# Kernel optimization log

Hardware: AMD Instinct MI355X
Metric: run time of the kernel (lower is better)

## Reference

```python
import jax, jax.numpy as jnp
import numpy as np

N_NODES = 100000
N_EDGES = 1600000
N_IN = 256
N_H = 128


def setup_inputs() -> dict:
    key = jax.random.key(0)
    k1, k2, k3, k4 = jax.random.split(key, 4)
    x = jax.random.normal(k1, (N_NODES, N_IN), dtype=jnp.float32)
    edge_index = jax.random.randint(k2, (2, N_EDGES), 0, N_NODES, dtype=jnp.int64)
    # GCNConv weights (glorot-like scale) and biases
    W1 = jax.random.normal(k3, (N_IN, N_H), dtype=jnp.float32) / np.sqrt(N_IN)
    b1 = jnp.zeros((N_H,), dtype=jnp.float32)
    W2 = jax.random.normal(k4, (N_H, N_H), dtype=jnp.float32) / np.sqrt(N_H)
    b2 = jnp.zeros((N_H,), dtype=jnp.float32)
    return {"x": x, "W1": W1, "b1": b1, "W2": W2, "b2": b2, "edge_index": edge_index}


def _gcn_conv(x, W, b, row, col, n_nodes):
    """PyG GCNConv: add self-loops, symmetric norm D^-1/2 A D^-1/2, aggregate at target (col)."""
    h = x @ W  # [N, out]
    # degree including self-loop (edge_weight = 1): deg[i] = 1 + #incoming edges at target i
    deg = jnp.ones((n_nodes,), dtype=x.dtype).at[col].add(1.0)
    dinv = jax.lax.rsqrt(deg)
    # off-diagonal edges: msg j->i weighted by dinv[j]*dinv[i]
    norm = dinv[row] * dinv[col]  # [E]
    msg = h[row] * norm[:, None]  # [E, out]
    agg = jax.ops.segment_sum(msg, col, num_segments=n_nodes)
    # self-loop contribution: weight dinv[i]^2
    agg = agg + h * (dinv * dinv)[:, None]
    return agg + b


def reference(x, W1, b1, W2, b2, edge_index):
    row, col = edge_index[0], edge_index[1]
    n = x.shape[0]
    out = jax.nn.relu(_gcn_conv(x, W1, b1, row, col, n))
    out = _gcn_conv(out, W2, b2, row, col, n)
    return out
```

## Files before the change

### kernel.cpp

```cpp
#include <hip/hip_runtime.h>


#define NN 100000
#define NH 128
#define NB 196
#define SB 256

__device__ __forceinline__ float bf2f(unsigned int u) { return __uint_as_float(u << 16); }
__device__ __forceinline__ unsigned short f2bf(float f) {
    unsigned int u = __float_as_uint(f);
    u = (u + 0x7fffu + ((u >> 16) & 1u)) >> 16;
    return (unsigned short)u;
}

__device__ __forceinline__ void dma16(const void* g, void* l) {
    __builtin_amdgcn_global_load_lds(
        (const __attribute__((address_space(1))) unsigned int*)g,
        (__attribute__((address_space(3))) unsigned int*)l, 16, 0, 0);
}

__global__ __launch_bounds__(256) void k_hist(const int* __restrict__ col,
                                              int* __restrict__ blockCnt, int E, int chb) {
    __shared__ int h[NB];
    int t = threadIdx.x, blk = blockIdx.x;
    if (t < NB) h[t] = 0;
    __syncthreads();
    int s = blk * chb, en = min(E, s + chb);
    for (int e = s + t; e < en; e += 256) atomicAdd(&h[col[e] >> 9], 1);
    __syncthreads();
    if (t < NB) blockCnt[t * SB + blk] = h[t];
}

__global__ __launch_bounds__(256) void k_base(const int* __restrict__ blockCnt,
                                              int* __restrict__ base) {
    __shared__ int s[256];
    int t = threadIdx.x;
    int tot = 0;
    if (t < NB)
        for (int j = 0; j < SB; ++j) tot += blockCnt[t * SB + j];
    s[t] = tot;
    __syncthreads();
    for (int off = 1; off < 256; off <<= 1) {
        int v = (t >= off) ? s[t - off] : 0;
        __syncthreads();
        s[t] += v;
        __syncthreads();
    }
    if (t < NB) base[t] = s[t] - tot;
    if (t == NB - 1) base[NB] = s[t];
}

__global__ __launch_bounds__(256) void k_bscan(const int* __restrict__ blockCnt,
                                               const int* __restrict__ base,
                                               int* __restrict__ blockOff) {
    __shared__ int s[256];
    int t = threadIdx.x, b = blockIdx.x;
    int v = blockCnt[b * SB + t];
    s[t] = v;
    __syncthreads();
    for (int off = 1; off < 256; off <<= 1) {
        int u = (t >= off) ? s[t - off] : 0;
        __syncthreads();
        s[t] += u;
        __syncthreads();
    }
    blockOff[b * SB + t] = base[b] + s[t] - v;
}

__global__ __launch_bounds__(256) void k_scatter(const int* __restrict__ row,
                                                 const int* __restrict__ col,
                                                 const int* __restrict__ blockOff,
                                                 unsigned int* __restrict__ pairs,
                                                 int E, int chb) {
    __shared__ int cur[NB];
    __shared__ int bof[NB];
    int t = threadIdx.x, blk = blockIdx.x;
    if (t < NB) {
        cur[t] = 0;
        bof[t] = blockOff[t * SB + blk];
    }
    __syncthreads();
    int s = blk * chb, en = min(E, s + chb);
    for (int e = s + t; e < en; e += 256) {
        int c = col[e];
        int b = c >> 9;
        int r = atomicAdd(&cur[b], 1);
        pairs[bof[b] + r] = (unsigned int)row[e] | ((unsigned int)(c & 511) << 17);
    }
}

__global__ __launch_bounds__(512) void k_bin(const unsigned int* __restrict__ pairs,
                                             const int* __restrict__ base,
                                             unsigned int* __restrict__ csr,
                                             int* __restrict__ offs,
                                             float* __restrict__ dinv, int n) {
    __shared__ int cnt[512];
    __shared__ int s[512];
    int t = threadIdx.x, b = blockIdx.x;
    cnt[t] = 0;
    __syncthreads();
    int e0 = base[b], e1 = base[b + 1];
    for (int i = e0 + t; i < e1; i += 512) atomicAdd(&cnt[pairs[i] >> 17], 1);
    __syncthreads();
    int v = cnt[t];
    int node = b * 512 + t;
    if (node < n) dinv[node] = rsqrtf(1.0f + (float)v);
    s[t] = v;
    __syncthreads();
    for (int off = 1; off < 512; off <<= 1) {
        int u = (t >= off) ? s[t - off] : 0;
        __syncthreads();
        s[t] += u;
        __syncthreads();
    }
    int excl = s[t] - v;
    if (node <= n) offs[node] = e0 + excl;
    __syncthreads();
    cnt[t] = e0 + excl;
    __syncthreads();
    for (int i = e0 + t; i < e1; i += 512) {
        unsigned int p = pairs[i];
        int d = atomicAdd(&cnt[p >> 17], 1);
        csr[d] = p & 0x1FFFFu;
    }
}

__global__ void k_wprep(const float* __restrict__ W, unsigned short* __restrict__ T, int K) {
    int idx = blockIdx.x * 256 + threadIdx.x;
    if (idx >= K * 128) return;
    int k = idx >> 7, c = idx & 127;
    T[(size_t)c * K + k] = f2bf(W[idx]);
}

template <int K>
__global__ __launch_bounds__(256) void k_gemm_mfma(const float* __restrict__ A,
                                                   const unsigned short* __restrict__ Bt,
                                                   const float* __restrict__ dinv,
                                                   unsigned short* __restrict__ C, int M) {
    using bf16x8 = __attribute__((ext_vector_type(8))) short;
    using f32x4  = __attribute__((ext_vector_type(4))) float;
    constexpr int T = K / 32;
    __shared__ uint4 sA[2][1024];
    __shared__ uint4 sB[2][512];

    const int lane = threadIdx.x & 63;
    const int wv   = threadIdx.x >> 6;
    const int r    = lane & 15;
    const int kb   = lane >> 4;
    const int rowBase = blockIdx.x * 128;

    auto stage = [&](int ks, int b) {
        const int kk = ks * 32;
#pragma unroll
        for (int c = 0; c < 4; ++c) {
            int sb = wv * 256 + c * 64;
            int q  = sb + lane;
            int row = q >> 3, pg = (q & 7) ^ (row & 7);
            int gr = rowBase + row; if (gr >= M) gr = M - 1;
            dma16(A + (size_t)gr * K + kk + pg * 4, &sA[b][sb]);
        }
#pragma unroll
        for (int c = 0; c < 2; ++c) {
            int sb = wv * 128 + c * 64;
            int q  = sb + lane;
            int bc = q >> 2, pg = (q & 3) ^ (bc & 3);
            dma16(Bt + (size_t)bc * K + kk + pg * 8, &sB[b][sb]);
        }
    };

    f32x4 acc[2][8];
#pragma unroll
    for (int m = 0; m < 2; ++m)
#pragma unroll
        for (int t = 0; t < 8; ++t) acc[m][t] = (f32x4){0.f, 0.f, 0.f, 0.f};

    stage(0, 0);
    __syncthreads();
#pragma unroll
    for (int ks = 0; ks < T; ++ks) {
        const int buf = ks & 1;
        if (ks + 1 < T) stage(ks + 1, buf ^ 1);
        bf16x8 ah[2];
#pragma unroll
        for (int m = 0; m < 2; ++m) {
            int rowl = wv * 32 + m * 16 + r;
            int p0 = (2 * kb)     ^ (rowl & 7);
            int p1 = (2 * kb + 1) ^ (rowl & 7);
            uint4 u0 = sA[buf][rowl * 8 + p0];
            uint4 u1 = sA[buf][rowl * 8 + p1];
            float f[8];
            *(uint4*)&f[0] = u0;
            *(uint4*)&f[4] = u1;
#pragma unroll
            for (int j = 0; j < 8; ++j) ah[m][j] = (short)f2bf(f[j]);
        }
#pragma unroll
        for (int t = 0; t < 8; ++t) {
            int bc = t * 16 + r;
            bf16x8 bh = *(const bf16x8*)&sB[buf][bc * 4 + (kb ^ (bc & 3))];
#pragma unroll
            for (int m = 0; m < 2; ++m)
                acc[m][t] = __builtin_amdgcn_mfma_f32_16x16x32_bf16(ah[m], bh, acc[m][t], 0, 0, 0);
        }
        __syncthreads();
    }
    const int wrow = rowBase + wv * 32;
#pragma unroll
    for (int m = 0; m < 2; ++m) {
#pragma unroll
        for (int q = 0; q < 4; ++q) {
            int orow = wrow + m * 16 + kb * 4 + q;
            if (orow < M) {
                float dv = dinv[orow];
#pragma unroll
                for (int t = 0; t < 8; ++t)
                    C[(size_t)orow * 128 + t * 16 + r] = f2bf(acc[m][t][q] * dv);
            }
        }
    }
}

template <int K>
__global__ __launch_bounds__(256) void k_gemm_bf16(const unsigned short* __restrict__ A,
                                                   const unsigned short* __restrict__ Bt,
                                                   const float* __restrict__ dinv,
                                                   unsigned short* __restrict__ C, int M) {
    using bf16x8 = __attribute__((ext_vector_type(8))) short;
    using f32x4  = __attribute__((ext_vector_type(4))) float;
    constexpr int T = K / 32;
    __shared__ uint4 sA[2][512];
    __shared__ uint4 sB[2][512];

    const int lane = threadIdx.x & 63;
    const int wv   = threadIdx.x >> 6;
    const int r    = lane & 15;
    const int kb   = lane >> 4;
    const int rowBase = blockIdx.x * 128;

    auto stage = [&](int ks, int b) {
        const int kk = ks * 32;
#pragma unroll
        for (int c = 0; c < 2; ++c) {
            int sb = wv * 128 + c * 64;
            int q  = sb + lane;
            int row = q >> 2, pg = (q & 3) ^ (row & 3);
            int gr = rowBase + row; if (gr >= M) gr = M - 1;
            dma16(A + (size_t)gr * K + kk + pg * 8, &sA[b][sb]);
        }
#pragma unroll
        for (int c = 0; c < 2; ++c) {
            int sb = wv * 128 + c * 64;
            int q  = sb + lane;
            int bc = q >> 2, pg = (q & 3) ^ (bc & 3);
            dma16(Bt + (size_t)bc * K + kk + pg * 8, &sB[b][sb]);
        }
    };

    f32x4 acc[2][8];
#pragma unroll
    for (int m = 0; m < 2; ++m)
#pragma unroll
        for (int t = 0; t < 8; ++t) acc[m][t] = (f32x4){0.f, 0.f, 0.f, 0.f};

    stage(0, 0);
    __syncthreads();
#pragma unroll
    for (int ks = 0; ks < T; ++ks) {
        const int buf = ks & 1;
        if (ks + 1 < T) stage(ks + 1, buf ^ 1);
        bf16x8 a[2];
#pragma unroll
        for (int m = 0; m < 2; ++m) {
            int rowl = wv * 32 + m * 16 + r;
            a[m] = *(const bf16x8*)&sA[buf][rowl * 4 + (kb ^ (rowl & 3))];
        }
#pragma unroll
        for (int t = 0; t < 8; ++t) {
            int bc = t * 16 + r;
            bf16x8 bh = *(const bf16x8*)&sB[buf][bc * 4 + (kb ^ (bc & 3))];
#pragma unroll
            for (int m = 0; m < 2; ++m)
                acc[m][t] = __builtin_amdgcn_mfma_f32_16x16x32_bf16(a[m], bh, acc[m][t], 0, 0, 0);
        }
        __syncthreads();
    }
    const int wrow = rowBase + wv * 32;
#pragma unroll
    for (int m = 0; m < 2; ++m) {
#pragma unroll
        for (int q = 0; q < 4; ++q) {
            int orow = wrow + m * 16 + kb * 4 + q;
            if (orow < M) {
                float dv = dinv[orow];
#pragma unroll
                for (int t = 0; t < 8; ++t)
                    C[(size_t)orow * 128 + t * 16 + r] = f2bf(acc[m][t][q] * dv);
            }
        }
    }
}

#define ACC8(u)                                              \
    a[0] += bf2f(u.x & 0xffffu); a[1] += bf2f(u.x >> 16);    \
    a[2] += bf2f(u.y & 0xffffu); a[3] += bf2f(u.y >> 16);    \
    a[4] += bf2f(u.z & 0xffffu); a[5] += bf2f(u.z >> 16);    \
    a[6] += bf2f(u.w & 0xffffu); a[7] += bf2f(u.w >> 16);

template <bool RELU, bool BF16OUT>
__global__ __launch_bounds__(256) void k_agg(const unsigned short* __restrict__ hb,
                                             const float* __restrict__ dinv,
                                             const int* __restrict__ off,
                                             const unsigned int* __restrict__ csr,
                                             const float* __restrict__ bias,
                                             void* __restrict__ outv, int n) {
    int gid  = blockIdx.x * 256 + threadIdx.x;
    int node = gid >> 4;
    int lane = gid & 15;
    if (node >= n) return;
    float di = dinv[node];
    uint4 us = *(const uint4*)(hb + ((size_t)node << 7) + lane * 8);
    float a[8];
    a[0] = bf2f(us.x & 0xffffu); a[1] = bf2f(us.x >> 16);
    a[2] = bf2f(us.y & 0xffffu); a[3] = bf2f(us.y >> 16);
    a[4] = bf2f(us.z & 0xffffu); a[5] = bf2f(us.z >> 16);
    a[6] = bf2f(us.w & 0xffffu); a[7] = bf2f(us.w >> 16);
    int e  = off[node];
    int e1 = off[node + 1];
    for (; e + 8 <= e1; e += 8) {
        unsigned int s0 = csr[e + 0], s1 = csr[e + 1], s2 = csr[e + 2], s3 = csr[e + 3];
        unsigned int s4 = csr[e + 4], s5 = csr[e + 5], s6 = csr[e + 6], s7 = csr[e + 7];
        uint4 u0 = *(const uint4*)(hb + ((size_t)s0 << 7) + lane * 8);
        uint4 u1 = *(const uint4*)(hb + ((size_t)s1 << 7) + lane * 8);
        uint4 u2 = *(const uint4*)(hb + ((size_t)s2 << 7) + lane * 8);
        uint4 u3 = *(const uint4*)(hb + ((size_t)s3 << 7) + lane * 8);
        uint4 u4 = *(const uint4*)(hb + ((size_t)s4 << 7) + lane * 8);
        uint4 u5 = *(const uint4*)(hb + ((size_t)s5 << 7) + lane * 8);
        uint4 u6 = *(const uint4*)(hb + ((size_t)s6 << 7) + lane * 8);
        uint4 u7 = *(const uint4*)(hb + ((size_t)s7 << 7) + lane * 8);
        ACC8(u0) ACC8(u1) ACC8(u2) ACC8(u3) ACC8(u4) ACC8(u5) ACC8(u6) ACC8(u7)
    }
    for (; e + 4 <= e1; e += 4) {
        unsigned int s0 = csr[e + 0], s1 = csr[e + 1], s2 = csr[e + 2], s3 = csr[e + 3];
        uint4 u0 = *(const uint4*)(hb + ((size_t)s0 << 7) + lane * 8);
        uint4 u1 = *(const uint4*)(hb + ((size_t)s1 << 7) + lane * 8);
        uint4 u2 = *(const uint4*)(hb + ((size_t)s2 << 7) + lane * 8);
        uint4 u3 = *(const uint4*)(hb + ((size_t)s3 << 7) + lane * 8);
        ACC8(u0) ACC8(u1) ACC8(u2) ACC8(u3)
    }
    for (; e < e1; ++e) {
        unsigned int s = csr[e];
        uint4 u = *(const uint4*)(hb + ((size_t)s << 7) + lane * 8);
        ACC8(u)
    }
    float4 b0 = *(const float4*)&bias[lane * 8];
    float4 b1 = *(const float4*)&bias[lane * 8 + 4];
    a[0] = a[0] * di + b0.x; a[1] = a[1] * di + b0.y;
    a[2] = a[2] * di + b0.z; a[3] = a[3] * di + b0.w;
    a[4] = a[4] * di + b1.x; a[5] = a[5] * di + b1.y;
    a[6] = a[6] * di + b1.z; a[7] = a[7] * di + b1.w;
    if (RELU) {
#pragma unroll
        for (int j = 0; j < 8; ++j) a[j] = fmaxf(a[j], 0.f);
    }
    if (BF16OUT) {
        uint4 o;
        o.x = (unsigned int)f2bf(a[0]) | ((unsigned int)f2bf(a[1]) << 16);
        o.y = (unsigned int)f2bf(a[2]) | ((unsigned int)f2bf(a[3]) << 16);
        o.z = (unsigned int)f2bf(a[4]) | ((unsigned int)f2bf(a[5]) << 16);
        o.w = (unsigned int)f2bf(a[6]) | ((unsigned int)f2bf(a[7]) << 16);
        *(uint4*)((unsigned short*)outv + ((size_t)node << 7) + lane * 8) = o;
    } else {
        float* op = (float*)outv + ((size_t)node << 7) + lane * 8;
        *(float4*)op       = make_float4(a[0], a[1], a[2], a[3]);
        *(float4*)(op + 4) = make_float4(a[4], a[5], a[6], a[7]);
    }
}

extern "C" void kernel_launch(void* const* d_in, const int* in_sizes, int n_in,
                              void* d_out, int out_size, void* d_ws, size_t ws_size,
                              hipStream_t stream) {
    const float* x  = (const float*)d_in[0];
    const float* W1 = (const float*)d_in[1];
    const float* b1 = (const float*)d_in[2];
    const float* W2 = (const float*)d_in[3];
    const float* b2 = (const float*)d_in[4];
    const int*   ei = (const int*)d_in[5];

    const int n = NN;
    const int E = in_sizes[5] / 2;
    const int* row = ei;
    const int* col = ei + E;

    char* ws = (char*)d_ws;
    size_t o = 0;
    auto alloc = [&](size_t bytes) {
        void* p = ws + o;
        o = (o + bytes + 255) & ~(size_t)255;
        return p;
    };
    int*            blockCnt = (int*)alloc((size_t)NB * SB * 4);
    int*            blockOff = (int*)alloc((size_t)NB * SB * 4);
    int*            base     = (int*)alloc((size_t)(NB + 1) * 4);
    int*            offs     = (int*)alloc((size_t)(n + 1) * 4);
    float*          dinv     = (float*)alloc((size_t)n * 4);
    unsigned int*   pairs    = (unsigned int*)alloc((size_t)E * 4);
    unsigned int*   csr      = (unsigned int*)alloc((size_t)E * 4);
    unsigned short* bufH     = (unsigned short*)alloc((size_t)n * NH * 2);
    unsigned short* bufG     = (unsigned short*)alloc((size_t)n * NH * 2);
    unsigned short* wt1      = (unsigned short*)alloc(256 * 128 * 2);
    unsigned short* wt2      = (unsigned short*)alloc(128 * 128 * 2);

    const int chb = (E + SB - 1) / SB;

    k_wprep<<<(256 * 128 + 255) / 256, 256, 0, stream>>>(W1, wt1, 256);
    k_wprep<<<(128 * 128 + 255) / 256, 256, 0, stream>>>(W2, wt2, 128);

    k_hist<<<SB, 256, 0, stream>>>(col, blockCnt, E, chb);
    k_base<<<1, 256, 0, stream>>>(blockCnt, base);
    k_bscan<<<NB, 256, 0, stream>>>(blockCnt, base, blockOff);
    k_scatter<<<SB, 256, 0, stream>>>(row, col, blockOff, pairs, E, chb);
    k_bin<<<NB, 512, 0, stream>>>(pairs, base, csr, offs, dinv, n);

    int aggBlocks = (n + 15) / 16;
    int gemmBlocks = (n + 127) / 128;
    k_gemm_mfma<256><<<gemmBlocks, 256, 0, stream>>>(x, wt1, dinv, bufH, n);
    k_agg<true, true><<<aggBlocks, 256, 0, stream>>>(bufH, dinv, offs, csr, b1, bufG, n);
    k_gemm_bf16<128><<<gemmBlocks, 256, 0, stream>>>(bufG, wt2, dinv, bufH, n);
    k_agg<false, false><<<aggBlocks, 256, 0, stream>>>(bufH, dinv, offs, csr, b2, d_out, n);
}
```

Measured before the change: 227.8 us.

## Reorder second GCN layer to aggregate-then-multiply and fuse aggregation with GEMM

Uses associativity to aggregate the first layer's ReLU output (pre-scaled by dinv) before multiplying by W2. This lets the second aggregation and the 128x128 GEMM run in one kernel: each block gathers 128 nodes into LDS as bf16, then runs MFMA against W2 read straight from global memory. The standalone bf16 GEMM kernel goes away, along with its intermediate write and read, and the two weight-prep launches are merged into one. Each fused block now does 128 nodes of gathering at lower parallelism (16 threads per node, 8 passes), which could hurt latency hiding. The final output also gains an extra bf16 rounding of the aggregated features before the GEMM.

```diff
diff --git a/kernel.cpp b/kernel.cpp
--- a/kernel.cpp
+++ b/kernel.cpp
@@ -125,11 +125,19 @@
     }
 }
 
-__global__ void k_wprep(const float* __restrict__ W, unsigned short* __restrict__ T, int K) {
+__global__ void k_wprep2(const float* __restrict__ W1, const float* __restrict__ W2,
+                         unsigned short* __restrict__ T1, unsigned short* __restrict__ T2) {
     int idx = blockIdx.x * 256 + threadIdx.x;
-    if (idx >= K * 128) return;
-    int k = idx >> 7, c = idx & 127;
-    T[(size_t)c * K + k] = f2bf(W[idx]);
+    if (idx < 256 * 128) {
+        int k = idx >> 7, c = idx & 127;
+        T1[(size_t)c * 256 + k] = f2bf(W1[idx]);
+    } else {
+        int j = idx - 256 * 128;
+        if (j < 128 * 128) {
+            int k = j >> 7, c = j & 127;
+            T2[(size_t)c * 128 + k] = f2bf(W2[j]);
+        }
+    }
 }
 
 template <int K>
@@ -220,105 +228,52 @@
     }
 }
 
-template <int K>
-__global__ __launch_bounds__(256) void k_gemm_bf16(const unsigned short* __restrict__ A,
-                                                   const unsigned short* __restrict__ Bt,
-                                                   const float* __restrict__ dinv,
-                                                   unsigned short* __restrict__ C, int M) {
-    using bf16x8 = __attribute__((ext_vector_type(8))) short;
-    using f32x4  = __attribute__((ext_vector_type(4))) float;
-    constexpr int T = K / 32;
-    __shared__ uint4 sA[2][512];
-    __shared__ uint4 sB[2][512];
-
-    const int lane = threadIdx.x & 63;
-    const int wv   = threadIdx.x >> 6;
-    const int r    = lane & 15;
-    const int kb   = lane >> 4;
-    const int rowBase = blockIdx.x * 128;
-
-    auto stage = [&](int ks, int b) {
-        const int kk = ks * 32;
-#pragma unroll
-        for (int c = 0; c < 2; ++c) {
-            int sb = wv * 128 + c * 64;
-            int q  = sb + lane;
-            int row = q >> 2, pg = (q & 3) ^ (row & 3);
-            int gr = rowBase + row; if (gr >= M) gr = M - 1;
-            dma16(A + (size_t)gr * K + kk + pg * 8, &sA[b][sb]);
-        }
-#pragma unroll
-        for (int c = 0; c < 2; ++c) {
-            int sb = wv * 128 + c * 64;
-            int q  = sb + lane;
-            int bc = q >> 2, pg = (q & 3) ^ (bc & 3);
-            dma16(Bt + (size_t)bc * K + kk + pg * 8, &sB[b][sb]);
-        }
-    };
-
-    f32x4 acc[2][8];
-#pragma unroll
-    for (int m = 0; m < 2; ++m)
-#pragma unroll
-        for (int t = 0; t < 8; ++t) acc[m][t] = (f32x4){0.f, 0.f, 0.f, 0.f};
-
-    stage(0, 0);
-    __syncthreads();
-#pragma unroll
-    for (int ks = 0; ks < T; ++ks) {
-        const int buf = ks & 1;
-        if (ks + 1 < T) stage(ks + 1, buf ^ 1);
-        bf16x8 a[2];
-#pragma unroll
-        for (int m = 0; m < 2; ++m) {
-            int rowl = wv * 32 + m * 16 + r;
-            a[m] = *(const bf16x8*)&sA[buf][rowl * 4 + (kb ^ (rowl & 3))];
-        }
-#pragma unroll
-        for (int t = 0; t < 8; ++t) {
-            int bc = t * 16 + r;
-            bf16x8 bh = *(const bf16x8*)&sB[buf][bc * 4 + (kb ^ (bc & 3))];
-#pragma unroll
-            for (int m = 0; m < 2; ++m)
-                acc[m][t] = __builtin_amdgcn_mfma_f32_16x16x32_bf16(a[m], bh, acc[m][t], 0, 0, 0);
-        }
-        __syncthreads();
-    }
-    const int wrow = rowBase + wv * 32;
-#pragma unroll
-    for (int m = 0; m < 2; ++m) {
-#pragma unroll
-        for (int q = 0; q < 4; ++q) {
-            int orow = wrow + m * 16 + kb * 4 + q;
-            if (orow < M) {
-                float dv = dinv[orow];
-#pragma unroll
-                for (int t = 0; t < 8; ++t)
-                    C[(size_t)orow * 128 + t * 16 + r] = f2bf(acc[m][t][q] * dv);
-            }
-        }
-    }
-}
-
 #define ACC8(u)                                              \
     a[0] += bf2f(u.x & 0xffffu); a[1] += bf2f(u.x >> 16);    \
     a[2] += bf2f(u.y & 0xffffu); a[3] += bf2f(u.y >> 16);    \
     a[4] += bf2f(u.z & 0xffffu); a[5] += bf2f(u.z >> 16);    \
     a[6] += bf2f(u.w & 0xffffu); a[7] += bf2f(u.w >> 16);
 
-template <bool RELU, bool BF16OUT>
-__global__ __launch_bounds__(256) void k_agg(const unsigned short* __restrict__ hb,
-                                             const float* __restrict__ dinv,
-                                             const int* __restrict__ off,
-                                             const unsigned int* __restrict__ csr,
-                                             const float* __restrict__ bias,
-                                             void* __restrict__ outv, int n) {
+#define GATHER_EDGES(hbp)                                                      \
+    for (; e + 8 <= e1; e += 8) {                                              \
+        unsigned int s0 = csr[e + 0], s1 = csr[e + 1], s2 = csr[e + 2], s3 = csr[e + 3]; \
+        unsigned int s4 = csr[e + 4], s5 = csr[e + 5], s6 = csr[e + 6], s7 = csr[e + 7]; \
+        uint4 u0 = *(const uint4*)(hbp + ((size_t)s0 << 7) + l16 * 8);         \
+        uint4 u1 = *(const uint4*)(hbp + ((size_t)s1 << 7) + l16 * 8);         \
+        uint4 u2 = *(const uint4*)(hbp + ((size_t)s2 << 7) + l16 * 8);         \
+        uint4 u3 = *(const uint4*)(hbp + ((size_t)s3 << 7) + l16 * 8);         \
+        uint4 u4 = *(const uint4*)(hbp + ((size_t)s4 << 7) + l16 * 8);         \
+        uint4 u5 = *(const uint4*)(hbp + ((size_t)s5 << 7) + l16 * 8);         \
+        uint4 u6 = *(const uint4*)(hbp + ((size_t)s6 << 7) + l16 * 8);         \
+        uint4 u7 = *(const uint4*)(hbp + ((size_t)s7 << 7) + l16 * 8);         \
+        ACC8(u0) ACC8(u1) ACC8(u2) ACC8(u3) ACC8(u4) ACC8(u5) ACC8(u6) ACC8(u7)\
+    }                                                                          \
+    for (; e + 4 <= e1; e += 4) {                                              \
+        unsigned int s0 = csr[e + 0], s1 = csr[e + 1], s2 = csr[e + 2], s3 = csr[e + 3]; \
+        uint4 u0 = *(const uint4*)(hbp + ((size_t)s0 << 7) + l16 * 8);         \
+        uint4 u1 = *(const uint4*)(hbp + ((size_t)s1 << 7) + l16 * 8);         \
+        uint4 u2 = *(const uint4*)(hbp + ((size_t)s2 << 7) + l16 * 8);         \
+        uint4 u3 = *(const uint4*)(hbp + ((size_t)s3 << 7) + l16 * 8);         \
+        ACC8(u0) ACC8(u1) ACC8(u2) ACC8(u3)                                    \
+    }                                                                          \
+    for (; e < e1; ++e) {                                                      \
+        unsigned int s = csr[e];                                               \
+        uint4 u = *(const uint4*)(hbp + ((size_t)s << 7) + l16 * 8);           \
+        ACC8(u)                                                                \
+    }
+
+__global__ __launch_bounds__(256) void k_agg1(const unsigned short* __restrict__ hb,
+                                              const float* __restrict__ dinv,
+                                              const int* __restrict__ off,
+                                              const unsigned int* __restrict__ csr,
+                                              const float* __restrict__ bias,
+                                              unsigned short* __restrict__ outg, int n) {
     int gid  = blockIdx.x * 256 + threadIdx.x;
     int node = gid >> 4;
-    int lane = gid & 15;
+    int l16  = gid & 15;
     if (node >= n) return;
     float di = dinv[node];
-    uint4 us = *(const uint4*)(hb + ((size_t)node << 7) + lane * 8);
+    uint4 us = *(const uint4*)(hb + ((size_t)node << 7) + l16 * 8);
     float a[8];
     a[0] = bf2f(us.x & 0xffffu); a[1] = bf2f(us.x >> 16);
     a[2] = bf2f(us.y & 0xffffu); a[3] = bf2f(us.y >> 16);
@@ -326,53 +281,109 @@
     a[6] = bf2f(us.w & 0xffffu); a[7] = bf2f(us.w >> 16);
     int e  = off[node];
     int e1 = off[node + 1];
-    for (; e + 8 <= e1; e += 8) {
-        unsigned int s0 = csr[e + 0], s1 = csr[e + 1], s2 = csr[e + 2], s3 = csr[e + 3];
-        unsigned int s4 = csr[e + 4], s5 = csr[e + 5], s6 = csr[e + 6], s7 = csr[e + 7];
-        uint4 u0 = *(const uint4*)(hb + ((size_t)s0 << 7) + lane * 8);
-        uint4 u1 = *(const uint4*)(hb + ((size_t)s1 << 7) + lane * 8);
-        uint4 u2 = *(const uint4*)(hb + ((size_t)s2 << 7) + lane * 8);
-        uint4 u3 = *(const uint4*)(hb + ((size_t)s3 << 7) + lane * 8);
-        uint4 u4 = *(const uint4*)(hb + ((size_t)s4 << 7) + lane * 8);
-        uint4 u5 = *(const uint4*)(hb + ((size_t)s5 << 7) + lane * 8);
-        uint4 u6 = *(const uint4*)(hb + ((size_t)s6 << 7) + lane * 8);
-        uint4 u7 = *(const uint4*)(hb + ((size_t)s7 << 7) + lane * 8);
-        ACC8(u0) ACC8(u1) ACC8(u2) ACC8(u3) ACC8(u4) ACC8(u5) ACC8(u6) ACC8(u7)
-    }
-    for (; e + 4 <= e1; e += 4) {
-        unsigned int s0 = csr[e + 0], s1 = csr[e + 1], s2 = csr[e + 2], s3 = csr[e + 3];
-        uint4 u0 = *(const uint4*)(hb + ((size_t)s0 << 7) + lane * 8);
-        uint4 u1 = *(const uint4*)(hb + ((size_t)s1 << 7) + lane * 8);
-        uint4 u2 = *(const uint4*)(hb + ((size_t)s2 << 7) + lane * 8);
-        uint4 u3 = *(const uint4*)(hb + ((size_t)s3 << 7) + lane * 8);
-        ACC8(u0) ACC8(u1) ACC8(u2) ACC8(u3)
-    }
-    for (; e < e1; ++e) {
-        unsigned int s = csr[e];
-        uint4 u = *(const uint4*)(hb + ((size_t)s << 7) + lane * 8);
-        ACC8(u)
-    }
-    float4 b0 = *(const float4*)&bias[lane * 8];
-    float4 b1 = *(const float4*)&bias[lane * 8 + 4];
-    a[0] = a[0] * di + b0.x; a[1] = a[1] * di + b0.y;
-    a[2] = a[2] * di + b0.z; a[3] = a[3] * di + b0.w;
-    a[4] = a[4] * di + b1.x; a[5] = a[5] * di + b1.y;
-    a[6] = a[6] * di + b1.z; a[7] = a[7] * di + b1.w;
-    if (RELU) {
-#pragma unroll
-        for (int j = 0; j < 8; ++j) a[j] = fmaxf(a[j], 0.f);
-    }
-    if (BF16OUT) {
-        uint4 o;
-        o.x = (unsigned int)f2bf(a[0]) | ((unsigned int)f2bf(a[1]) << 16);
-        o.y = (unsigned int)f2bf(a[2]) | ((unsigned int)f2bf(a[3]) << 16);
-        o.z = (unsigned int)f2bf(a[4]) | ((unsigned int)f2bf(a[5]) << 16);
-        o.w = (unsigned int)f2bf(a[6]) | ((unsigned int)f2bf(a[7]) << 16);
-        *(uint4*)((unsigned short*)outv + ((size_t)node << 7) + lane * 8) = o;
-    } else {
-        float* op = (float*)outv + ((size_t)node << 7) + lane * 8;
-        *(float4*)op       = make_float4(a[0], a[1], a[2], a[3]);
-        *(float4*)(op + 4) = make_float4(a[4], a[5], a[6], a[7]);
+    GATHER_EDGES(hb)
+    float4 b0 = *(const float4*)&bias[l16 * 8];
+    float4 b1 = *(const float4*)&bias[l16 * 8 + 4];
+    a[0] = fmaxf(a[0] * di + b0.x, 0.f) * di;
+    a[1] = fmaxf(a[1] * di + b0.y, 0.f) * di;
+    a[2] = fmaxf(a[2] * di + b0.z, 0.f) * di;
+    a[3] = fmaxf(a[3] * di + b0.w, 0.f) * di;
+    a[4] = fmaxf(a[4] * di + b1.x, 0.f) * di;
+    a[5] = fmaxf(a[5] * di + b1.y, 0.f) * di;
+    a[6] = fmaxf(a[6] * di + b1.z, 0.f) * di;
+    a[7] = fmaxf(a[7] * di + b1.w, 0.f) * di;
+    uint4 o;
+    o.x = (unsigned int)f2bf(a[0]) | ((unsigned int)f2bf(a[1]) << 16);
+    o.y = (unsigned int)f2bf(a[2]) | ((unsigned int)f2bf(a[3]) << 16);
+    o.z = (unsigned int)f2bf(a[4]) | ((unsigned int)f2bf(a[5]) << 16);
+    o.w = (unsigned int)f2bf(a[6]) | ((unsigned int)f2bf(a[7]) << 16);
+    *(uint4*)(outg + ((size_t)node << 7) + l16 * 8) = o;
+}
+
+__global__ __launch_bounds__(256) void k_aggmm(const unsigned short* __restrict__ gs,
+                                               const float* __restrict__ dinv,
+                                               const int* __restrict__ off,
+                                               const unsigned int* __restrict__ csr,
+                                               const unsigned short* __restrict__ Bt,
+                                               const float* __restrict__ bias,
+                                               float* __restrict__ out, int n) {
+    using bf16x8 = __attribute__((ext_vector_type(8))) short;
+    using f32x4  = __attribute__((ext_vector_type(4))) float;
+    __shared__ uint4 tl[128 * 16];
+
+    const int tid  = threadIdx.x;
+    const int nb0  = blockIdx.x * 128;
+
+    {
+        int grp = tid >> 4;
+        int l16 = tid & 15;
+        for (int nl = 0; nl < 8; ++nl) {
+            int rowl = nl * 16 + grp;
+            int node = nb0 + rowl;
+            float a[8] = {0.f, 0.f, 0.f, 0.f, 0.f, 0.f, 0.f, 0.f};
+            if (node < n) {
+                uint4 us = *(const uint4*)(gs + ((size_t)node << 7) + l16 * 8);
+                a[0] = bf2f(us.x & 0xffffu); a[1] = bf2f(us.x >> 16);
+                a[2] = bf2f(us.y & 0xffffu); a[3] = bf2f(us.y >> 16);
+                a[4] = bf2f(us.z & 0xffffu); a[5] = bf2f(us.z >> 16);
+                a[6] = bf2f(us.w & 0xffffu); a[7] = bf2f(us.w >> 16);
+                int e  = off[node];
+                int e1 = off[node + 1];
+                GATHER_EDGES(gs)
+                float di = dinv[node];
+#pragma unroll
+                for (int j = 0; j < 8; ++j) a[j] *= di;
+            }
+            uint4 o;
+            o.x = (unsigned int)f2bf(a[0]) | ((unsigned int)f2bf(a[1]) << 16);
+            o.y = (unsigned int)f2bf(a[2]) | ((unsigned int)f2bf(a[3]) << 16);
+            o.z = (unsigned int)f2bf(a[4]) | ((unsigned int)f2bf(a[5]) << 16);
+            o.w = (unsigned int)f2bf(a[6]) | ((unsigned int)f2bf(a[7]) << 16);
+            tl[rowl * 16 + (l16 ^ (rowl & 15))] = o;
+        }
+    }
+    __syncthreads();
+    const int lane = tid & 63;
+    const int wv   = tid >> 6;
+    const int r    = lane & 15;
+    const int kb   = lane >> 4;
+
+    f32x4 acc[2][8];
+#pragma unroll
+    for (int m = 0; m < 2; ++m)
+#pragma unroll
+        for (int t = 0; t < 8; ++t) acc[m][t] = (f32x4){0.f, 0.f, 0.f, 0.f};
+
+#pragma unroll
+    for (int ks = 0; ks < 4; ++ks) {
+        bf16x8 a[2];
+#pragma unroll
+        for (int m = 0; m < 2; ++m) {
+            int rowl = wv * 32 + m * 16 + r;
+            int pidx = ks * 4 + kb;
+            a[m] = *(const bf16x8*)&tl[rowl * 16 + (pidx ^ (rowl & 15))];
+        }
+#pragma unroll
+        for (int t = 0; t < 8; ++t) {
+            int bc = t * 16 + r;
+            bf16x8 bh = *(const bf16x8*)(Bt + (size_t)bc * 128 + ks * 32 + kb * 8);
+#pragma unroll
+            for (int m = 0; m < 2; ++m)
+                acc[m][t] = __builtin_amdgcn_mfma_f32_16x16x32_bf16(a[m], bh, acc[m][t], 0, 0, 0);
+        }
+    }
+    const int wrow = nb0 + wv * 32;
+#pragma unroll
+    for (int m = 0; m < 2; ++m) {
+#pragma unroll
+        for (int q = 0; q < 4; ++q) {
+            int orow = wrow + m * 16 + kb * 4 + q;
+            if (orow < n) {
+#pragma unroll
+                for (int t = 0; t < 8; ++t)
+                    out[(size_t)orow * 128 + t * 16 + r] = acc[m][t][q] + bias[t * 16 + r];
+            }
+        }
     }
 }
 
@@ -412,8 +423,7 @@
 
     const int chb = (E + SB - 1) / SB;
 
-    k_wprep<<<(256 * 128 + 255) / 256, 256, 0, stream>>>(W1, wt1, 256);
-    k_wprep<<<(128 * 128 + 255) / 256, 256, 0, stream>>>(W2, wt2, 128);
+    k_wprep2<<<(384 * 128 + 255) / 256, 256, 0, stream>>>(W1, W2, wt1, wt2);
 
     k_hist<<<SB, 256, 0, stream>>>(col, blockCnt, E, chb);
     k_base<<<1, 256, 0, stream>>>(blockCnt, base);
@@ -421,10 +431,9 @@
     k_scatter<<<SB, 256, 0, stream>>>(row, col, blockOff, pairs, E, chb);
     k_bin<<<NB, 512, 0, stream>>>(pairs, base, csr, offs, dinv, n);
 
-    int aggBlocks = (n + 15) / 16;
+    int aggBlocks  = (n + 15) / 16;
     int gemmBlocks = (n + 127) / 128;
     k_gemm_mfma<256><<<gemmBlocks, 256, 0, stream>>>(x, wt1, dinv, bufH, n);
-    k_agg<true, true><<<aggBlocks, 256, 0, stream>>>(bufH, dinv, offs, csr, b1, bufG, n);
-    k_gemm_bf16<128><<<gemmBlocks, 256, 0, stream>>>(bufG, wt2, dinv, bufH, n);
-    k_agg<false, false><<<aggBlocks, 256, 0, stream>>>(bufH, dinv, offs, csr, b2, d_out, n);
-}
+    k_agg1<<<aggBlocks, 256, 0, stream>>>(bufH, dinv, offs, csr, b1, bufG, n);
+    k_aggmm<<<gemmBlocks, 256, 0, stream>>>(bufG, dinv, offs, csr, wt2, b2, (float*)d_out, n);
+}
```

Result: slower. 256.5 us (+12.6%).
